# Kernel optimization log

Measured on AMD Instinct MI355X. Metric: run time of the kernel, lower is better.

The kernel has to match this reference:

```python
import jax, jax.numpy as jnp
import numpy as np
from jax import lax

EPS = 1e-8

def _norm(v, eps=EPS):
    # matches torch F.normalize: v / max(||v||, eps)
    return v / jnp.maximum(jnp.linalg.norm(v, axis=-1, keepdims=True), eps)

def keep_r6(r6):
    v1 = _norm(r6[..., :3])
    v2 = r6[..., 3:6]
    v2 = v2 - jnp.sum(v2 * v1, axis=-1, keepdims=True) * v1
    v2n = jnp.linalg.norm(v2, axis=-1, keepdims=True)
    mask = (v2n < 1e-6).astype(r6.dtype)
    e1 = jnp.array([1.0, 0.0, 0.0], dtype=r6.dtype)
    e2 = jnp.array([0.0, 1.0, 0.0], dtype=r6.dtype)
    dot = jnp.abs(jnp.sum(v1 * e1, axis=-1, keepdims=True))
    fb = jnp.where(dot < 0.9, e1, e2)
    fb_v2 = jnp.cross(v1, jnp.broadcast_to(fb, v1.shape), axis=-1)
    v2 = (1.0 - mask) * v2 + mask * fb_v2
    v2 = _norm(v2)
    return jnp.concatenate([v1, v2], axis=-1)

def r6_to_matrix(r6):
    r6 = keep_r6(r6)
    v1, v2 = r6[..., :3], r6[..., 3:6]
    v3 = jnp.cross(v1, v2, axis=-1)
    R = jnp.stack([v1, v2, v3], axis=-1)  # columns v1,v2,v3
    det = jnp.linalg.det(R)
    return R * jnp.sign(det)[..., None, None]

def instance_norm(x, eps=1e-5):
    # InstanceNorm3d, affine=False: per-(B,C) stats over spatial dims, biased var
    mu = jnp.mean(x, axis=(2, 3, 4), keepdims=True)
    var = jnp.mean((x - mu) ** 2, axis=(2, 3, 4), keepdims=True)
    return (x - mu) * lax.rsqrt(var + eps)

def conv1x1(x, w, b):
    return jnp.einsum('oc,bcdhw->bodhw', w[:, :, 0, 0, 0], x) + b[None, :, None, None, None]

def conv3_circ(x, w, b):
    xp = jnp.pad(x, ((0, 0), (0, 0), (1, 1), (1, 1), (1, 1)), mode='wrap')
    out = lax.conv_general_dilated(xp, w, (1, 1, 1), 'VALID',
                                   dimension_numbers=('NCDHW', 'OIDHW', 'NCDHW'))
    return out + b[None, :, None, None, None]

def _gelu(t):
    return jax.nn.gelu(t, approximate=False)

def _forward(x, pos_emb, qkv_w, qkv_b, lp1_w, lp1_b, lp2_w, lp2_b,
             mod1_w, mod1_b, mod2_w, mod2_b, pa_w, pa_b,
             R6_d, R6_h, R6_w, proj_w, proj_b):
    B, C, D, H, W = x.shape
    NH = pa_w.shape[0]
    HD = C // NH
    NV = HD // 3
    scale = HD ** (-0.5)

    # PositionalProcessing (deterministic; computed once, reused for all 3 axes)
    local = conv1x1(_gelu(instance_norm(conv3_circ(pos_emb, lp1_w, lp1_b))), lp2_w, lp2_b)
    mod = jax.nn.sigmoid(conv1x1(_gelu(instance_norm(conv1x1(local, mod1_w, mod1_b))), mod2_w, mod2_b))
    x_mod = x * mod
    pos_attn = _gelu(instance_norm(conv1x1(pos_emb, pa_w, pa_b)))  # [B,NH,D,H,W]

    axes = [
        (R6_d, (0, 3, 4, 1, 2), (0, 4, 3, 1, 2)),  # depth
        (R6_h, (0, 2, 4, 1, 3), (0, 4, 1, 3, 2)),  # height
        (R6_w, (0, 2, 3, 1, 4), (0, 4, 1, 2, 3)),  # width
    ]
    out_sum = 0.0
    for R6, perm, inv in axes:
        xp = jnp.transpose(x_mod, perm)      # [B, A1, A2, C, L]
        Bb, A1, A2, _, L = xp.shape
        bd = Bb * A1 * A2
        xl = jnp.swapaxes(xp.reshape(bd, C, L), -1, -2)  # [bd, L, C]
        qkv = (xl @ qkv_w.T + qkv_b).reshape(bd, L, 3, NH, HD)
        qkv = jnp.transpose(qkv, (2, 0, 3, 1, 4))
        q, k, v = qkv[0], qkv[1], qkv[2]     # [bd, NH, L, HD]
        R = r6_to_matrix(keep_r6(R6))[0]     # [NH, 3, 3]

        def rot(t):
            tv = t.reshape(bd, NH, L, NV, 3)
            return jnp.einsum('hij,bhlvj->bhlvi', R, tv).reshape(bd, NH, L, HD)

        attn = jnp.einsum('bhqd,bhkd->bhqk', rot(q), rot(k)) * scale
        pa = jnp.transpose(pos_attn, perm).reshape(bd, NH, L)
        attn = jax.nn.softmax(attn + pa[..., None], axis=-1)
        o = jnp.einsum('bhqk,bhkd->bhqd', attn, v)      # [bd, NH, L, HD]
        o = jnp.swapaxes(o, 1, 2).reshape(Bb, A1, A2, L, C)
        out_sum = out_sum + jnp.transpose(o, inv)        # [B, C, D, H, W]
    return conv1x1(out_sum, proj_w, proj_b)


def setup_inputs() -> dict:
    key = jax.random.key(0)
    ks = jax.random.split(key, 20)
    B, C, D, H, W, NH = 2, 96, 40, 40, 40, 4

    def rn(k, shape, s=0.05):
        return jax.random.normal(k, shape, dtype=jnp.float32) * s

    return {
        'x': jax.random.normal(ks[0], (B, C, D, H, W), dtype=jnp.float32),
        'pos_emb': jax.random.normal(ks[1], (B, C, D, H, W), dtype=jnp.float32),
        'qkv_w': rn(ks[2], (3 * C, C)), 'qkv_b': rn(ks[3], (3 * C,)),
        'lp1_w': rn(ks[4], (C, C, 3, 3, 3)), 'lp1_b': rn(ks[5], (C,)),
        'lp2_w': rn(ks[6], (C, C, 1, 1, 1)), 'lp2_b': rn(ks[7], (C,)),
        'mod1_w': rn(ks[8], (C, C, 1, 1, 1)), 'mod1_b': rn(ks[9], (C,)),
        'mod2_w': rn(ks[10], (C, C, 1, 1, 1)), 'mod2_b': rn(ks[11], (C,)),
        'pa_w': rn(ks[12], (NH, C, 1, 1, 1)), 'pa_b': rn(ks[13], (NH,)),
        'R6_d': jax.random.normal(ks[14], (1, NH, 6), dtype=jnp.float32),
        'R6_h': jax.random.normal(ks[15], (1, NH, 6), dtype=jnp.float32),
        'R6_w': jax.random.normal(ks[16], (1, NH, 6), dtype=jnp.float32),
        'proj_w': rn(ks[17], (C, C, 1, 1, 1)), 'proj_b': rn(ks[18], (C,)),
    }


def reference(x, pos_emb, qkv_w, qkv_b, lp1_w, lp1_b, lp2_w, lp2_b,
              mod1_w, mod1_b, mod2_w, mod2_b, pa_w, pa_b,
              R6_d, R6_h, R6_w, proj_w, proj_b):
    return _forward(x, pos_emb, qkv_w, qkv_b, lp1_w, lp1_b, lp2_w, lp2_b,
                    mod1_w, mod1_b, mod2_w, mod2_b, pa_w, pa_b,
                    R6_d, R6_h, R6_w, proj_w, proj_b)
```

## Files before the change

kernel.cpp:

```cpp
#include <hip/hip_runtime.h>


typedef __attribute__((ext_vector_type(8))) _Float16 half8;
typedef __attribute__((ext_vector_type(2))) _Float16 half2;
typedef __attribute__((ext_vector_type(16))) float floatx16;

static __device__ __forceinline__ half2 h2(unsigned int u) {
    return __builtin_bit_cast(half2, u);
}
static __device__ __forceinline__ float fdot2(unsigned int a, unsigned int b, float c) {
    return __builtin_amdgcn_fdot2(h2(a), h2(b), c, false);
}

__global__ void k_zero(float* __restrict__ p) {
    int t = threadIdx.x;
    for (int i = t; i < 768; i += 256) p[i] = 0.f;
}

__global__ __launch_bounds__(256) void k_cvt_in(const float* __restrict__ pos,
                                                _Float16* __restrict__ in_t) {
    __shared__ _Float16 lds[64][97];
    int bid = blockIdx.x;
    int xcd = bid & 7, k = bid >> 3;
    int L;
    if (xcd < 4) L = xcd * 63 + (k >> 2);
    else { if (k >= 248) return; L = 252 + (xcd - 4) * 62 + (k >> 2); }
    int q = k & 3;
    int b = L / 250;
    int s0 = (L % 250) * 256 + q * 64;
    int t = threadIdx.x;
    for (int i = t; i < 6144; i += 256) {
        int c = i / 64, sl = i % 64;
        lds[sl][c] = (_Float16)pos[(b * 96 + c) * 64000 + s0 + sl];
    }
    __syncthreads();
    _Float16* outp = in_t + ((size_t)b * 64000 + s0) * 96;
    for (int i = t; i < 6144; i += 256) {
        int sl = i / 96, c = i % 96;
        outp[i] = lds[sl][c];
    }
}

__global__ void k_cvt_w(const float* __restrict__ w, _Float16* __restrict__ wf) {
    int i = blockIdx.x * 256 + threadIdx.x;
    if (i < 248832) {
        int c = i % 96, m = (i / 96) % 96, tap = i / 9216;
        wf[i] = (_Float16)w[(m * 96 + c) * 27 + tap];
    }
}

__global__ void k_cvt_f16(const float* __restrict__ w, _Float16* __restrict__ o, int n) {
    int i = blockIdx.x * 256 + threadIdx.x;
    if (i < n) o[i] = (_Float16)w[i];
}

__global__ __launch_bounds__(256) void k_fold(const float* __restrict__ lp2_w,
                                              const float* __restrict__ lp2_b,
                                              const float* __restrict__ mod1_w,
                                              const float* __restrict__ mod1_b,
                                              _Float16* __restrict__ wfold,
                                              float* __restrict__ bfold) {
    int i = blockIdx.x * 256 + threadIdx.x;
    if (i < 9216) {
        int o = i / 96, c = i % 96;
        float a = 0.f;
        for (int k = 0; k < 96; k++) a += mod1_w[o * 96 + k] * lp2_w[k * 96 + c];
        wfold[i] = (_Float16)a;
    }
    if (blockIdx.x == 0 && threadIdx.x < 96) {
        int o = threadIdx.x;
        float a = mod1_b[o];
        for (int k = 0; k < 96; k++) a += mod1_w[o * 96 + k] * lp2_b[k];
        bfold[o] = a;
    }
}

__global__ __launch_bounds__(256) void k_conv3_v2(const _Float16* __restrict__ in_t,
                                                  const _Float16* __restrict__ wf,
                                                  const float* __restrict__ bias,
                                                  _Float16* __restrict__ c3) {
    __shared__ int tbl[27 * 256];
    __shared__ _Float16 st[256 * 98];
    __shared__ float bsh[96];
    int t = threadIdx.x;
    int bid = blockIdx.x;
    {
        int xcd = bid & 7, idx = bid >> 3;
        bid = (xcd < 4) ? (xcd * 63 + idx) : (252 + (xcd - 4) * 62 + idx);
    }
    int b = bid / 250;
    int s0 = (bid % 250) * 256;

    for (int u = t; u < 27 * 256; u += 256) {
        int tap = u >> 8, nl = u & 255;
        int kd = tap / 9, kh = (tap / 3) % 3, kw = tap % 3;
        int s = s0 + nl;
        int d = s / 1600, r = s - d * 1600;
        int h = r / 40, w = r - h * 40;
        int ds = d + kd - 1; if (ds < 0) ds += 40; else if (ds >= 40) ds -= 40;
        int hs = h + kh - 1; if (hs < 0) hs += 40; else if (hs >= 40) hs -= 40;
        int wv2 = w + kw - 1; if (wv2 < 0) wv2 += 40; else if (wv2 >= 40) wv2 -= 40;
        tbl[u] = ((ds * 1600 + hs * 40 + wv2) * 96) * 2;
    }
    if (t < 96) bsh[t] = bias[t];
    __syncthreads();

    int wv = t >> 6, lane = t & 63;
    int n31 = lane & 31, kg = lane >> 5;
    const char* inb = (const char*)(in_t + (size_t)b * 64000 * 96) + kg * 16;

    floatx16 acc[3][2];
#pragma unroll
    for (int mt = 0; mt < 3; mt++)
#pragma unroll
        for (int nt = 0; nt < 2; nt++)
#pragma unroll
            for (int r = 0; r < 16; r++) acc[mt][nt][r] = 0.f;

    for (int tap = 0; tap < 27; tap++) {
        int ta0 = tbl[tap * 256 + wv * 64 + n31];
        int ta1 = tbl[tap * 256 + wv * 64 + 32 + n31];
        const char* pb0 = inb + ta0;
        const char* pb1 = inb + ta1;
        const _Float16* wt = wf + tap * 9216 + kg * 8;
#pragma unroll
        for (int j = 0; j < 6; j++) {
            half8 a0 = *(const half8*)(wt + (n31) * 96 + j * 16);
            half8 a1 = *(const half8*)(wt + (32 + n31) * 96 + j * 16);
            half8 a2 = *(const half8*)(wt + (64 + n31) * 96 + j * 16);
            half8 b0 = *(const half8*)(pb0 + j * 32);
            half8 b1 = *(const half8*)(pb1 + j * 32);
            acc[0][0] = __builtin_amdgcn_mfma_f32_32x32x16_f16(a0, b0, acc[0][0], 0, 0, 0);
            acc[0][1] = __builtin_amdgcn_mfma_f32_32x32x16_f16(a0, b1, acc[0][1], 0, 0, 0);
            acc[1][0] = __builtin_amdgcn_mfma_f32_32x32x16_f16(a1, b0, acc[1][0], 0, 0, 0);
            acc[1][1] = __builtin_amdgcn_mfma_f32_32x32x16_f16(a1, b1, acc[1][1], 0, 0, 0);
            acc[2][0] = __builtin_amdgcn_mfma_f32_32x32x16_f16(a2, b0, acc[2][0], 0, 0, 0);
            acc[2][1] = __builtin_amdgcn_mfma_f32_32x32x16_f16(a2, b1, acc[2][1], 0, 0, 0);
        }
    }

#pragma unroll
    for (int mt = 0; mt < 3; mt++)
#pragma unroll
        for (int nt = 0; nt < 2; nt++)
#pragma unroll
            for (int r = 0; r < 16; r++) {
                int m = mt * 32 + (r & 3) + 8 * (r >> 2) + 4 * kg;
                int sl = wv * 64 + nt * 32 + n31;
                st[sl * 98 + m] = (_Float16)(acc[mt][nt][r] + bsh[m]);
            }
    __syncthreads();

    unsigned int* dst = (unsigned int*)(c3 + ((size_t)(b * 64000 + s0)) * 96);
    for (int i = t; i < 12288; i += 256) {
        int row = i / 48, sg = i % 48;
        dst[i] = *(const unsigned int*)&st[row * 98 + sg * 2];
    }
}

__global__ __launch_bounds__(192) void k_stats_sc(const _Float16* __restrict__ in,
                                                  float* __restrict__ raw) {
    __shared__ float red_s[16][96], red_q[16][96];
    int bid = blockIdx.x;
    int b = bid / 50, ch = bid % 50;
    int t = threadIdx.x;
    int sp = t / 12, cs = t % 12;
    const uint4* base = (const uint4*)(in + ((size_t)(b * 64000 + ch * 1280)) * 96);
    float s8[8], q8[8];
#pragma unroll
    for (int e = 0; e < 8; e++) { s8[e] = 0.f; q8[e] = 0.f; }
    for (int i = 0; i < 80; i++) {
        uint4 v = base[(sp + i * 16) * 12 + cs];
        half8 h = __builtin_bit_cast(half8, v);
#pragma unroll
        for (int e = 0; e < 8; e++) { float f = (float)h[e]; s8[e] += f; q8[e] += f * f; }
    }
#pragma unroll
    for (int e = 0; e < 8; e++) { red_s[sp][cs * 8 + e] = s8[e]; red_q[sp][cs * 8 + e] = q8[e]; }
    __syncthreads();
    if (t < 96) {
        float S = 0.f, Q = 0.f;
        for (int k = 0; k < 16; k++) { S += red_s[k][t]; Q += red_q[k][t]; }
        atomicAdd(&raw[(b * 96 + t) * 2], S);
        atomicAdd(&raw[(b * 96 + t) * 2 + 1], Q);
    }
}

__global__ void k_finalize(const float* __restrict__ raw, float2* __restrict__ sf) {
    int t = threadIdx.x;
    if (t < 192) {
        float S = raw[t * 2], Q = raw[t * 2 + 1];
        float mu = S * (1.f / 64000.f);
        float var = Q * (1.f / 64000.f) - mu * mu;
        sf[t] = make_float2(mu, rsqrtf(var + 1e-5f));
    }
}

__global__ __launch_bounds__(256) void k_ng16(_Float16* __restrict__ x, const float2* __restrict__ sf) {
    int t = threadIdx.x, bid = blockIdx.x;
    uint4* p = (uint4*)x;
#pragma unroll
    for (int k = 0; k < 4; k++) {
        int i = bid * 1024 + k * 256 + t;
        int e0 = i * 8;
        int b = e0 / 6144000;
        int c0 = e0 % 96;
        const float2* sp = &sf[b * 96 + c0];
        uint4 v = p[i];
        half8 h = __builtin_bit_cast(half8, v);
        _Float16 o[8];
#pragma unroll
        for (int e = 0; e < 8; e++) {
            float2 st = sp[e];
            float u = ((float)h[e] - st.x) * st.y;
            o[e] = (_Float16)(0.5f * u * (1.f + erff(u * 0.70710678118654752f)));
        }
        p[i] = *(uint4*)o;
    }
}

template <int MODE>
__global__ __launch_bounds__(256) void k_gemm96(const _Float16* __restrict__ in,
                                                const _Float16* __restrict__ w,
                                                const float* __restrict__ bias,
                                                const float* __restrict__ xg,
                                                _Float16* __restrict__ outp) {
    __shared__ _Float16 un[12544];
    __shared__ float bias_s[96];
    int t = threadIdx.x, bid = blockIdx.x;
    { int xcd = bid & 7; bid = xcd * 125 + (bid >> 3); }
    int b = bid / 500, s0 = (bid % 500) * 128;
    for (int i = t; i < 1152; i += 256) ((uint4*)un)[i] = ((const uint4*)w)[i];
    if (t < 96) bias_s[t] = bias[t];
    __syncthreads();

    int ws = t >> 6, lane = t & 63;
    int n = lane & 31, kg = lane >> 5;
    int p = ws * 32 + n;
    const uint4* brow = (const uint4*)(in + ((size_t)(b * 64000 + s0 + p)) * 96);
    uint4 bf[6];
#pragma unroll
    for (int kc = 0; kc < 6; kc++) bf[kc] = brow[kc * 2 + kg];

    floatx16 acc[3];
#pragma unroll
    for (int mt = 0; mt < 3; mt++)
#pragma unroll
        for (int r = 0; r < 16; r++) acc[mt][r] = 0.f;
#pragma unroll
    for (int kc = 0; kc < 6; kc++) {
        half8 bfh = __builtin_bit_cast(half8, bf[kc]);
#pragma unroll
        for (int mt = 0; mt < 3; mt++) {
            uint4 au = *(const uint4*)&un[(mt * 32 + n) * 96 + kc * 16 + kg * 8];
            acc[mt] = __builtin_amdgcn_mfma_f32_32x32x16_f16(__builtin_bit_cast(half8, au), bfh, acc[mt], 0, 0, 0);
        }
    }
    __syncthreads();

#pragma unroll
    for (int mt = 0; mt < 3; mt++)
#pragma unroll
        for (int r = 0; r < 16; r++) {
            int m = mt * 32 + (r & 3) + 8 * (r >> 2) + 4 * kg;
            int sl = ws * 32 + n;
            float v = acc[mt][r] + bias_s[m];
            if (MODE == 1) {
                v = 1.f / (1.f + __expf(-v));
                v *= xg[((size_t)(b * 96 + m)) * 64000 + s0 + sl];
            }
            un[sl * 98 + m] = (_Float16)v;
        }
    __syncthreads();

    unsigned int* dst = (unsigned int*)(outp + ((size_t)(b * 64000 + s0)) * 96);
    for (int i = t; i < 6144; i += 256) {
        int row = i / 48, sg = i % 48;
        dst[i] = *(const unsigned int*)&un[row * 98 + sg * 2];
    }
}

__global__ __launch_bounds__(256) void k_qkv(const _Float16* __restrict__ xt,
                                             const _Float16* __restrict__ wq,
                                             const float* __restrict__ qb,
                                             _Float16* __restrict__ qA) {
    __shared__ _Float16 smem[27648];
    __shared__ float bias_s[288];
    int t = threadIdx.x;
    int bid = blockIdx.x;
    { int xcd = bid & 7; bid = xcd * 125 + (bid >> 3); }
    int b = bid / 500;
    int s0 = (bid % 500) * 128;

    for (int i = t; i < 3456; i += 256) ((uint4*)smem)[i] = ((const uint4*)wq)[i];
    for (int i = t; i < 288; i += 256) bias_s[i] = qb[i];
    __syncthreads();

    int ws = t >> 6, lane = t & 63;
    int n = lane & 31, kg = lane >> 5;
    int p = ws * 32 + n;

    const uint4* brow = (const uint4*)(xt + ((size_t)(b * 64000 + s0 + p)) * 96);
    uint4 bf[6];
#pragma unroll
    for (int kc = 0; kc < 6; kc++) bf[kc] = brow[kc * 2 + kg];

    floatx16 acc[9];
#pragma unroll
    for (int mt = 0; mt < 9; mt++)
#pragma unroll
        for (int r = 0; r < 16; r++) acc[mt][r] = 0.f;

#pragma unroll
    for (int kc = 0; kc < 6; kc++) {
        half8 bfh = __builtin_bit_cast(half8, bf[kc]);
#pragma unroll
        for (int mt = 0; mt < 9; mt++) {
            uint4 au = *(const uint4*)&smem[(mt * 32 + n) * 96 + kc * 16 + kg * 8];
            acc[mt] = __builtin_amdgcn_mfma_f32_32x32x16_f16(__builtin_bit_cast(half8, au), bfh, acc[mt], 0, 0, 0);
        }
    }

    const float scale = 0.20412414523193154f;
    for (int q = 0; q < 2; q++) {
        __syncthreads();
        if ((ws >> 1) == q) {
            int pl = (ws & 1) * 32 + n;
#pragma unroll
            for (int mt = 0; mt < 9; mt++)
#pragma unroll
                for (int g = 0; g < 4; g++) {
                    int m0 = mt * 32 + g * 8 + kg * 4;
                    _Float16 tm[4];
#pragma unroll
                    for (int j = 0; j < 4; j++) {
                        float v = acc[mt][g * 4 + j] + bias_s[m0 + j];
                        if (m0 + j < 96) v *= scale;
                        tm[j] = (_Float16)v;
                    }
                    *(uint2*)&smem[pl * 296 + m0] = *(uint2*)tm;
                }
        }
        __syncthreads();
        for (int idx = t; idx < 2304; idx += 256) {
            int pl = idx / 36, seg = idx % 36;
            int s = s0 + q * 64 + pl;
            uint4 v = *(const uint4*)&smem[pl * 296 + seg * 8];
            *(uint4*)&qA[((size_t)(b * 64000 + s)) * 288 + seg * 8] = v;
        }
    }
}

template <int AXIS, bool ACC>
__global__ __launch_bounds__(320, 3) void k_attn(const _Float16* __restrict__ qA,
                                                 _Float16* __restrict__ osum) {
    __shared__ _Float16 kk[8352];
    __shared__ _Float16 vT[7744];
    int t = threadIdx.x;
    int bid = blockIdx.x;
    bid = (bid & 7) * 200 + (bid >> 3);
    int b = bid / 800;
    int r0 = (bid % 800) * 2;

    auto smap = [&](int r, int l) -> int {
        if (AXIS == 0) return l * 1600 + r;
        else if (AXIS == 1) { int d = r / 40, w = r % 40; return d * 1600 + l * 40 + w; }
        else return r * 40 + l;
    };
    const uint4* src = (const uint4*)qA;
    for (int i = t; i < 960; i += 320) {
        int line = i / 480, key = (i % 480) / 12, seg = i % 12;
        int row = b * 64000 + smap(r0 + line, key);
        ((uint4*)kk)[i] = src[(size_t)row * 36 + 12 + seg];
    }
    for (int i = t; i < 960; i += 320) {
        int line = i / 480, key = (i % 480) / 12, seg = i % 12;
        int row = b * 64000 + smap(r0 + line, key);
        uint4 v = src[(size_t)row * 36 + 24 + seg];
        _Float16 tmp[8];
        *(uint4*)tmp = v;
#pragma unroll
        for (int e = 0; e < 8; e++) {
            int hdg = seg * 8 + e;
            vT[(line * 4 + hdg / 24) * 968 + (hdg % 24) * 40 + key] = tmp[e];
        }
    }

    int line = t / 160, head = (t % 160) / 40, ql = t % 40;
    int rr = r0 + line;
    unsigned int qu[12];
    {
        const uint4* qp = (const uint4*)(qA + ((size_t)(b * 64000 + smap(rr, ql))) * 288 + head * 24);
#pragma unroll
        for (int j = 0; j < 3; j++) *(uint4*)&qu[j * 4] = qp[j];
    }
    __syncthreads();

    float s[40];
    const uint4* kbase = (const uint4*)kk + line * 480 + head * 3;
#pragma unroll 4
    for (int key = 0; key < 40; key++) {
        unsigned int kku[12];
#pragma unroll
        for (int j = 0; j < 3; j++) *(uint4*)&kku[j * 4] = kbase[key * 12 + j];
        float a = 0.f;
#pragma unroll
        for (int i = 0; i < 12; i++) a = fdot2(kku[i], qu[i], a);
        s[key] = a;
    }

    float mx = -1e30f;
#pragma unroll
    for (int i = 0; i < 40; i++) mx = fmaxf(mx, s[i]);
    float sum = 0.f;
#pragma unroll
    for (int i = 0; i < 40; i++) { s[i] = __expf(s[i] - mx); sum += s[i]; }
    float inv = 1.f / sum;

    unsigned int pw[20];
#pragma unroll
    for (int i = 0; i < 20; i++) {
        half2 a = { (_Float16)(s[2 * i] * inv), (_Float16)(s[2 * i + 1] * inv) };
        pw[i] = __builtin_bit_cast(unsigned int, a);
    }

    __syncthreads();

    float o[24];
    const uint4* vbase = (const uint4*)vT + (line * 4 + head) * 121;
#pragma unroll 2
    for (int hd = 0; hd < 24; hd++) {
        unsigned int vv[20];
#pragma unroll
        for (int j = 0; j < 5; j++) *(uint4*)&vv[j * 4] = vbase[hd * 5 + j];
        float a = 0.f;
#pragma unroll
        for (int i = 0; i < 20; i++) a = fdot2(vv[i], pw[i], a);
        o[hd] = a;
    }

    {
        _Float16 tm[24];
#pragma unroll
        for (int j = 0; j < 24; j++) tm[j] = (_Float16)o[j];
        _Float16* dA = &kk[(line * 40 + ql) * 104 + head * 24];
#pragma unroll
        for (int j = 0; j < 3; j++) ((uint4*)dA)[j] = ((uint4*)tm)[j];
    }
    __syncthreads();

    uint4* dst = (uint4*)osum;
    for (int i = t; i < 960; i += 320) {
        int row = i / 12, seg = i % 12;
        int s2 = smap(r0 + row / 40, row % 40);
        size_t di = ((size_t)(b * 64000 + s2)) * 12 + seg;
        uint4 v = *(const uint4*)&kk[row * 104 + seg * 8];
        if (ACC) {
            half8 a = __builtin_bit_cast(half8, dst[di]);
            half8 c = __builtin_bit_cast(half8, v);
            dst[di] = __builtin_bit_cast(uint4, a + c);
        } else {
            dst[di] = v;
        }
    }
}

__global__ __launch_bounds__(256) void k_proj(const _Float16* __restrict__ osum,
                                              const _Float16* __restrict__ wp,
                                              const float* __restrict__ pb,
                                              float* __restrict__ out) {
    __shared__ _Float16 A[9216];
    __shared__ float bias_s[96];
    int t = threadIdx.x;
    int bid = blockIdx.x;
    int b = bid / 500;
    int s0 = (bid % 500) * 128;
    for (int i = t; i < 1152; i += 256) ((uint4*)A)[i] = ((const uint4*)wp)[i];
    if (t < 96) bias_s[t] = pb[t];
    __syncthreads();

    int ws = t >> 6, lane = t & 63;
    int n = lane & 31, kg = lane >> 5;
    int s = s0 + ws * 32 + n;

    const uint4* brow = (const uint4*)(osum + ((size_t)(b * 64000 + s0 + ws * 32 + n)) * 96);
    uint4 bf[6];
#pragma unroll
    for (int kc = 0; kc < 6; kc++) bf[kc] = brow[kc * 2 + kg];

    floatx16 acc[3];
#pragma unroll
    for (int mt = 0; mt < 3; mt++)
#pragma unroll
        for (int r = 0; r < 16; r++) acc[mt][r] = 0.f;

#pragma unroll
    for (int kc = 0; kc < 6; kc++) {
        half8 bfh = __builtin_bit_cast(half8, bf[kc]);
#pragma unroll
        for (int mt = 0; mt < 3; mt++) {
            uint4 au = *(const uint4*)&A[(mt * 32 + n) * 96 + kc * 16 + kg * 8];
            acc[mt] = __builtin_amdgcn_mfma_f32_32x32x16_f16(__builtin_bit_cast(half8, au), bfh, acc[mt], 0, 0, 0);
        }
    }

#pragma unroll
    for (int mt = 0; mt < 3; mt++)
#pragma unroll
        for (int r = 0; r < 16; r++) {
            int m = mt * 32 + (r & 3) + 8 * (r >> 2) + 4 * kg;
            out[((size_t)(b * 96 + m)) * 64000 + s] = acc[mt][r] + bias_s[m];
        }
}

extern "C" void kernel_launch(void* const* d_in, const int* in_sizes, int n_in,
                              void* d_out, int out_size, void* d_ws, size_t ws_size,
                              hipStream_t stream) {
    const float* x      = (const float*)d_in[0];
    const float* pos    = (const float*)d_in[1];
    const float* qkv_w  = (const float*)d_in[2];
    const float* qkv_b  = (const float*)d_in[3];
    const float* lp1_w  = (const float*)d_in[4];
    const float* lp1_b  = (const float*)d_in[5];
    const float* lp2_w  = (const float*)d_in[6];
    const float* lp2_b  = (const float*)d_in[7];
    const float* mod1_w = (const float*)d_in[8];
    const float* mod1_b = (const float*)d_in[9];
    const float* mod2_w = (const float*)d_in[10];
    const float* mod2_b = (const float*)d_in[11];
    const float* proj_w = (const float*)d_in[17];
    const float* proj_b = (const float*)d_in[18];
    float* out = (float*)d_out;
    float* ws = (float*)d_ws;

    _Float16* bufA = (_Float16*)ws;
    _Float16* bufB = (_Float16*)(ws + 6144000);
    _Float16* qA   = (_Float16*)(ws + 12288000);
    _Float16* in_t = qA;
    _Float16* wf   = (_Float16*)(ws + 30720000);
    _Float16* wq   = (_Float16*)(ws + 30844416);
    _Float16* wpj  = (_Float16*)(ws + 30858240);
    _Float16* wfold= (_Float16*)(ws + 30862848);
    _Float16* wm2  = (_Float16*)(ws + 30867456);
    float* bfold   = ws + 30872064;
    float* raw     = ws + 30872160;
    float2* sf0    = (float2*)(ws + 30872928);
    float2* sf1    = (float2*)(ws + 30873312);
    float* raw0 = raw, *raw1 = raw + 384;

    k_zero<<<1, 256, 0, stream>>>(raw);
    k_cvt_in<<<2016, 256, 0, stream>>>(pos, in_t);
    k_cvt_w<<<972, 256, 0, stream>>>(lp1_w, wf);
    k_fold<<<36, 256, 0, stream>>>(lp2_w, lp2_b, mod1_w, mod1_b, wfold, bfold);
    k_cvt_f16<<<36, 256, 0, stream>>>(mod2_w, wm2, 9216);
    k_cvt_f16<<<108, 256, 0, stream>>>(qkv_w, wq, 27648);
    k_cvt_f16<<<36, 256, 0, stream>>>(proj_w, wpj, 9216);

    k_conv3_v2<<<500, 256, 0, stream>>>(in_t, wf, lp1_b, bufA);
    k_stats_sc<<<100, 192, 0, stream>>>(bufA, raw0);
    k_finalize<<<1, 256, 0, stream>>>(raw0, sf0);
    k_ng16<<<1500, 256, 0, stream>>>(bufA, sf0);
    k_gemm96<0><<<1000, 256, 0, stream>>>(bufA, wfold, bfold, nullptr, bufB);
    k_stats_sc<<<100, 192, 0, stream>>>(bufB, raw1);
    k_finalize<<<1, 256, 0, stream>>>(raw1, sf1);
    k_ng16<<<1500, 256, 0, stream>>>(bufB, sf1);
    k_gemm96<1><<<1000, 256, 0, stream>>>(bufB, wm2, mod2_b, x, bufA);

    k_qkv<<<1000, 256, 0, stream>>>(bufA, wq, qkv_b, qA);
    k_attn<2, false><<<1600, 320, 0, stream>>>(qA, bufB);
    k_attn<0, true ><<<1600, 320, 0, stream>>>(qA, bufB);
    k_attn<1, true ><<<1600, 320, 0, stream>>>(qA, bufB);

    k_proj<<<1000, 256, 0, stream>>>(bufB, wpj, proj_b, out);
}
```

Measured before the change: 683.5 us.

## Stage conv3 weights in double-buffered LDS and fold tiny setup kernels

The 3x3x3 conv kernel now loads each tap's 96x96 fp16 weight slice into a padded, double-buffered LDS region. It prefetches the next tap into registers while the MFMAs run, instead of every wave reading weights straight from global memory. Separately, the zero-init kernel is merged into the weight conversion kernel, and the stats finalize kernel is folded into the normalize+GELU kernel, which recomputes mean/rstd per block into shared memory. This cuts launches and global weight traffic, but adds a block barrier per tap and a larger LDS footprint that may lower occupancy.

```diff
diff --git a/kernel.cpp b/kernel.cpp
--- a/kernel.cpp
+++ b/kernel.cpp
@@ -10,11 +10,6 @@
 }
 static __device__ __forceinline__ float fdot2(unsigned int a, unsigned int b, float c) {
     return __builtin_amdgcn_fdot2(h2(a), h2(b), c, false);
-}
-
-__global__ void k_zero(float* __restrict__ p) {
-    int t = threadIdx.x;
-    for (int i = t; i < 768; i += 256) p[i] = 0.f;
 }
 
 __global__ __launch_bounds__(256) void k_cvt_in(const float* __restrict__ pos,
@@ -41,11 +36,15 @@
     }
 }
 
-__global__ void k_cvt_w(const float* __restrict__ w, _Float16* __restrict__ wf) {
+__global__ void k_cvt_w(const float* __restrict__ w, _Float16* __restrict__ wf,
+                        float* __restrict__ raw) {
     int i = blockIdx.x * 256 + threadIdx.x;
     if (i < 248832) {
         int c = i % 96, m = (i / 96) % 96, tap = i / 9216;
         wf[i] = (_Float16)w[(m * 96 + c) * 27 + tap];
+    }
+    if (blockIdx.x == 0) {
+        for (int u = threadIdx.x; u < 768; u += 256) raw[u] = 0.f;
     }
 }
 
@@ -75,13 +74,16 @@
     }
 }
 
-__global__ __launch_bounds__(256) void k_conv3_v2(const _Float16* __restrict__ in_t,
+__global__ __launch_bounds__(256) void k_conv3_v6(const _Float16* __restrict__ in_t,
                                                   const _Float16* __restrict__ wf,
                                                   const float* __restrict__ bias,
                                                   _Float16* __restrict__ c3) {
-    __shared__ int tbl[27 * 256];
-    __shared__ _Float16 st[256 * 98];
-    __shared__ float bsh[96];
+    __shared__ __align__(16) char smem[67968];
+    int* tbl = (int*)smem;
+    char* Abuf = smem + 27648;
+    float* bsh = (float*)(smem + 67584);
+    _Float16* st = (_Float16*)smem;
+
     int t = threadIdx.x;
     int bid = blockIdx.x;
     {
@@ -103,6 +105,18 @@
         tbl[u] = ((ds * 1600 + hs * 40 + wv2) * 96) * 2;
     }
     if (t < 96) bsh[t] = bias[t];
+
+    {
+        const uint4* asrc = (const uint4*)wf;
+#pragma unroll
+        for (int k = 0; k < 5; k++) {
+            int i = k * 256 + t;
+            if (i < 1152) {
+                uint4 v = asrc[i];
+                *(uint4*)(Abuf + (i / 12) * 208 + (i % 12) * 16) = v;
+            }
+        }
+    }
     __syncthreads();
 
     int wv = t >> 6, lane = t & 63;
@@ -118,18 +132,28 @@
             for (int r = 0; r < 16; r++) acc[mt][nt][r] = 0.f;
 
     for (int tap = 0; tap < 27; tap++) {
+        int cur = tap & 1;
+        uint4 rA[5];
+        if (tap < 26) {
+            const uint4* asrc = (const uint4*)(wf + (tap + 1) * 9216);
+#pragma unroll
+            for (int k = 0; k < 5; k++) {
+                int i = k * 256 + t;
+                if (i < 1152) rA[k] = asrc[i];
+            }
+        }
         int ta0 = tbl[tap * 256 + wv * 64 + n31];
         int ta1 = tbl[tap * 256 + wv * 64 + 32 + n31];
         const char* pb0 = inb + ta0;
         const char* pb1 = inb + ta1;
-        const _Float16* wt = wf + tap * 9216 + kg * 8;
+        const char* Ac = Abuf + cur * 19968 + n31 * 208 + kg * 16;
 #pragma unroll
         for (int j = 0; j < 6; j++) {
-            half8 a0 = *(const half8*)(wt + (n31) * 96 + j * 16);
-            half8 a1 = *(const half8*)(wt + (32 + n31) * 96 + j * 16);
-            half8 a2 = *(const half8*)(wt + (64 + n31) * 96 + j * 16);
             half8 b0 = *(const half8*)(pb0 + j * 32);
             half8 b1 = *(const half8*)(pb1 + j * 32);
+            half8 a0 = *(const half8*)(Ac + j * 32);
+            half8 a1 = *(const half8*)(Ac + 32 * 208 + j * 32);
+            half8 a2 = *(const half8*)(Ac + 64 * 208 + j * 32);
             acc[0][0] = __builtin_amdgcn_mfma_f32_32x32x16_f16(a0, b0, acc[0][0], 0, 0, 0);
             acc[0][1] = __builtin_amdgcn_mfma_f32_32x32x16_f16(a0, b1, acc[0][1], 0, 0, 0);
             acc[1][0] = __builtin_amdgcn_mfma_f32_32x32x16_f16(a1, b0, acc[1][0], 0, 0, 0);
@@ -137,6 +161,15 @@
             acc[2][0] = __builtin_amdgcn_mfma_f32_32x32x16_f16(a2, b0, acc[2][0], 0, 0, 0);
             acc[2][1] = __builtin_amdgcn_mfma_f32_32x32x16_f16(a2, b1, acc[2][1], 0, 0, 0);
         }
+        if (tap < 26) {
+            char* Anx = Abuf + (cur ^ 1) * 19968;
+#pragma unroll
+            for (int k = 0; k < 5; k++) {
+                int i = k * 256 + t;
+                if (i < 1152) *(uint4*)(Anx + (i / 12) * 208 + (i % 12) * 16) = rA[k];
+            }
+        }
+        __syncthreads();
     }
 
 #pragma unroll
@@ -186,18 +219,16 @@
     }
 }
 
-__global__ void k_finalize(const float* __restrict__ raw, float2* __restrict__ sf) {
-    int t = threadIdx.x;
+__global__ __launch_bounds__(256) void k_ng16(_Float16* __restrict__ x, const float* __restrict__ raw) {
+    __shared__ float2 sfs[192];
+    int t = threadIdx.x, bid = blockIdx.x;
     if (t < 192) {
         float S = raw[t * 2], Q = raw[t * 2 + 1];
         float mu = S * (1.f / 64000.f);
         float var = Q * (1.f / 64000.f) - mu * mu;
-        sf[t] = make_float2(mu, rsqrtf(var + 1e-5f));
-    }
-}
-
-__global__ __launch_bounds__(256) void k_ng16(_Float16* __restrict__ x, const float2* __restrict__ sf) {
-    int t = threadIdx.x, bid = blockIdx.x;
+        sfs[t] = make_float2(mu, rsqrtf(var + 1e-5f));
+    }
+    __syncthreads();
     uint4* p = (uint4*)x;
 #pragma unroll
     for (int k = 0; k < 4; k++) {
@@ -205,7 +236,7 @@
         int e0 = i * 8;
         int b = e0 / 6144000;
         int c0 = e0 % 96;
-        const float2* sp = &sf[b * 96 + c0];
+        const float2* sp = &sfs[b * 96 + c0];
         uint4 v = p[i];
         half8 h = __builtin_bit_cast(half8, v);
         _Float16 o[8];
@@ -544,26 +575,21 @@
     _Float16* wm2  = (_Float16*)(ws + 30867456);
     float* bfold   = ws + 30872064;
     float* raw     = ws + 30872160;
-    float2* sf0    = (float2*)(ws + 30872928);
-    float2* sf1    = (float2*)(ws + 30873312);
     float* raw0 = raw, *raw1 = raw + 384;
 
-    k_zero<<<1, 256, 0, stream>>>(raw);
     k_cvt_in<<<2016, 256, 0, stream>>>(pos, in_t);
-    k_cvt_w<<<972, 256, 0, stream>>>(lp1_w, wf);
+    k_cvt_w<<<972, 256, 0, stream>>>(lp1_w, wf, raw);
     k_fold<<<36, 256, 0, stream>>>(lp2_w, lp2_b, mod1_w, mod1_b, wfold, bfold);
     k_cvt_f16<<<36, 256, 0, stream>>>(mod2_w, wm2, 9216);
     k_cvt_f16<<<108, 256, 0, stream>>>(qkv_w, wq, 27648);
     k_cvt_f16<<<36, 256, 0, stream>>>(proj_w, wpj, 9216);
 
-    k_conv3_v2<<<500, 256, 0, stream>>>(in_t, wf, lp1_b, bufA);
+    k_conv3_v6<<<500, 256, 0, stream>>>(in_t, wf, lp1_b, bufA);
     k_stats_sc<<<100, 192, 0, stream>>>(bufA, raw0);
-    k_finalize<<<1, 256, 0, stream>>>(raw0, sf0);
-    k_ng16<<<1500, 256, 0, stream>>>(bufA, sf0);
+    k_ng16<<<1500, 256, 0, stream>>>(bufA, raw0);
     k_gemm96<0><<<1000, 256, 0, stream>>>(bufA, wfold, bfold, nullptr, bufB);
     k_stats_sc<<<100, 192, 0, stream>>>(bufB, raw1);
-    k_finalize<<<1, 256, 0, stream>>>(raw1, sf1);
-    k_ng16<<<1500, 256, 0, stream>>>(bufB, sf1);
+    k_ng16<<<1500, 256, 0, stream>>>(bufB, raw1);
     k_gemm96<1><<<1000, 256, 0, stream>>>(bufB, wm2, mod2_b, x, bufA);
 
     k_qkv<<<1000, 256, 0, stream>>>(bufA, wq, qkv_b, qA);
```

Measured after the change: 719.4 us. +5.2%, slower.
